# Performance work log

Measured on AMD Instinct MI355X. Metric: run time of the kernel, lower is better.

Reference implementation:

```python
import jax, jax.numpy as jnp
import numpy as np

N_IN = 512    # input nodes occupy indices [0, N_IN)
N_OUT = 256   # output nodes are the last N_OUT node indices


def setup_inputs() -> dict:
    key = jax.random.key(0)
    ks = jax.random.split(key, 7)
    B, N, E = 32, 50000, 800000
    x = jax.random.normal(ks[0], (B, N_IN), dtype=jnp.float32)
    states = jax.random.normal(ks[1], (B, N), dtype=jnp.float32)
    # per-edge scalar weights (NEAT connection genes)
    weight = 0.1 * jax.random.normal(ks[2], (E,), dtype=jnp.float32)
    # per-node scalar bias / response (NEAT node genes)
    bias = 0.1 * jax.random.normal(ks[3], (N,), dtype=jnp.float32)
    response = 1.0 + 0.1 * jax.random.normal(ks[4], (N,), dtype=jnp.float32)
    edge_src = jax.random.randint(ks[5], (E,), 0, N, dtype=jnp.int64) if jax.config.jax_enable_x64 else jax.random.randint(ks[5], (E,), 0, N).astype(jnp.int32)
    edge_dst = jax.random.randint(ks[6], (E,), 0, N, dtype=jnp.int64) if jax.config.jax_enable_x64 else jax.random.randint(ks[6], (E,), 0, N).astype(jnp.int32)
    return {"x": x, "states": states, "weight": weight, "bias": bias,
            "response": response, "edge_src": edge_src, "edge_dst": edge_dst}


def reference(x, states, weight, bias, response, edge_src, edge_dst):
    """One recurrent step of a wired (NEAT-style) RNN.

    For every node i:  z_i = tanh(bias_i + response_i * sum_{(j->i)} w_ji * s_j)
    Input nodes are then clamped to the external input x; outputs are the
    activations of the last N_OUT nodes. Returns (y, new_states) like
    WiredRNN.forward.
    """
    B, N = states.shape
    # gather source states per edge and apply scalar edge weights: [B, E]
    contrib = states[:, edge_src] * weight
    # sum-aggregate incoming messages per destination node: [B, N]
    agg = jnp.zeros((B, N), dtype=states.dtype).at[:, edge_dst].add(contrib)
    z = jnp.tanh(bias + response * agg)
    new_states = z.at[:, :N_IN].set(x)  # input nodes carry the external input
    y = new_states[:, -N_OUT:]
    return (y, new_states)
```

## Files before the change

### kernel.cpp

```cpp
#include <hip/hip_runtime.h>


#define BATCH 32
#define N_IN 512
#define N_OUT 256
#define RB_LOG 6
#define RB 64
#define CAPL 2048
#define MAXR 2048
#define PCH 8192

static __device__ __forceinline__ unsigned short f2bf(float f) {
    unsigned u = __float_as_uint(f);
    unsigned r = (u + 0x7fffu + ((u >> 16) & 1u)) >> 16;
    return (unsigned short)r;
}

__global__ __launch_bounds__(1024)
void fpart_kernel(const float* __restrict__ s, unsigned short* __restrict__ sTb,
                  int N, int PB,
                  const int* __restrict__ edge_src,
                  const int* __restrict__ edge_dst,
                  const float* __restrict__ weight,
                  int* __restrict__ cursors,
                  int2* __restrict__ staging,
                  int E, int R, int CAP) {
    __shared__ int shbuf[4224];
    int tid = threadIdx.x;
    if ((int)blockIdx.x >= PB) {
        float* tiles = (float*)shbuf;
        int tx = tid & 31;
        int ty = tid >> 5;
        int nb = ((int)blockIdx.x - PB) * 128;
#pragma unroll
        for (int t = 0; t < 4; ++t) {
            int n = nb + t * 32 + tx;
            tiles[t * 1056 + ty * 33 + tx] =
                (n < N) ? s[(size_t)ty * N + n] : 0.f;
        }
        __syncthreads();
#pragma unroll
        for (int t = 0; t < 4; ++t) {
            int nn = nb + t * 32 + ty;
            if (nn < N)
                sTb[(size_t)nn * 32 + tx] = f2bf(tiles[t * 1056 + tx * 33 + ty]);
        }
        return;
    }
    int* h    = shbuf;
    int* lcur = shbuf + MAXR;
    for (int i = tid; i < R; i += 1024) h[i] = 0;
    __syncthreads();
    int e0 = blockIdx.x * PCH;
    int e1 = min(e0 + PCH, E);
    int dd[8], ss[8]; float ww[8];
#pragma unroll
    for (int it = 0; it < 2; ++it) {
        int e = e0 + it * 4096 + tid * 4;
#pragma unroll
        for (int j = 0; j < 4; ++j) dd[it * 4 + j] = -1;
        if (e + 4 <= e1) {
            int4 d4 = *reinterpret_cast<const int4*>(edge_dst + e);
            int4 s4 = *reinterpret_cast<const int4*>(edge_src + e);
            float4 w4 = *reinterpret_cast<const float4*>(weight + e);
            dd[it*4+0]=d4.x; dd[it*4+1]=d4.y; dd[it*4+2]=d4.z; dd[it*4+3]=d4.w;
            ss[it*4+0]=s4.x; ss[it*4+1]=s4.y; ss[it*4+2]=s4.z; ss[it*4+3]=s4.w;
            ww[it*4+0]=w4.x; ww[it*4+1]=w4.y; ww[it*4+2]=w4.z; ww[it*4+3]=w4.w;
        } else {
#pragma unroll
            for (int j = 0; j < 4; ++j) {
                if (e + j < e1) {
                    dd[it*4+j] = edge_dst[e + j];
                    ss[it*4+j] = edge_src[e + j];
                    ww[it*4+j] = weight[e + j];
                }
            }
        }
#pragma unroll
        for (int j = 0; j < 4; ++j) {
            int idx = it * 4 + j;
            if (dd[idx] >= N_IN) atomicAdd(&h[dd[idx] >> RB_LOG], 1);
        }
    }
    __syncthreads();
    for (int i = tid; i < R; i += 1024) {
        int c = h[i];
        lcur[i] = c ? (i * CAP + atomicAdd(&cursors[i], c)) : 0;
    }
    __syncthreads();
#pragma unroll
    for (int idx = 0; idx < 8; ++idx) {
        if (dd[idx] >= N_IN) {
            int rng = dd[idx] >> RB_LOG;
            int pos = atomicAdd(&lcur[rng], 1);
            if (pos < (rng + 1) * CAP)
                staging[pos] = make_int2(((dd[idx] & (RB - 1)) << 16) | ss[idx],
                                         __float_as_int(ww[idx]));
        }
    }
}

__global__ __launch_bounds__(512)
void accfin_kernel(const unsigned short* __restrict__ sTb,
                   const int2* __restrict__ staging,
                   const int* __restrict__ cursors,
                   const float* __restrict__ x,
                   const float* __restrict__ bias,
                   const float* __restrict__ response,
                   float* __restrict__ ns, float* __restrict__ y,
                   int N, int CAP) {
    __shared__ float acc[RB * 33];
    __shared__ int2  sorted[CAPL];
    __shared__ int   hstart[RB];
    __shared__ int   hcur[RB];
    int tid = threadIdx.x;
    int r = blockIdx.x;
    int base = r * RB;
    for (int i = tid; i < RB * 33; i += 512) acc[i] = 0.f;

    int b0 = r * CAP;
    int b1 = b0 + min(cursors[r], CAP);
    int q = tid & 7;
    int p = (tid >> 3) & 7;
    int wid = tid >> 6;
    int lane = tid & 63;

    for (int t = b0; t < b1; t += CAPL) {
        int m = min(CAPL, b1 - t);
        if (tid < RB) hstart[tid] = 0;
        __syncthreads();
        for (int i = tid; i < m; i += 512)
            atomicAdd(&hstart[((unsigned)staging[t + i].x) >> 16], 1);
        __syncthreads();
        if (tid < 64) {
            int v = hstart[lane];
            int incl = v;
#pragma unroll
            for (int off = 1; off < 64; off <<= 1) {
                int tv = __shfl_up(incl, off, 64);
                if (lane >= off) incl += tv;
            }
            hstart[lane] = incl - v;
            hcur[lane]   = incl - v;
        }
        __syncthreads();
        for (int i = tid; i < m; i += 512) {
            int2 rc = staging[t + i];
            int pos = atomicAdd(&hcur[((unsigned)rc.x) >> 16], 1);
            sorted[pos] = rc;
        }
        __syncthreads();
#pragma unroll
        for (int k = 0; k < 8; ++k) {
            int nl = wid * 8 + k;
            int beg = hstart[nl], end = hcur[nl];
            float a0 = 0.f, a1 = 0.f, a2 = 0.f, a3 = 0.f;
            for (int e = beg + p; e < end; e += 8) {
                int2 rc = sorted[e];
                float w = __int_as_float(rc.y);
                uint2 u2 = *reinterpret_cast<const uint2*>(
                    sTb + (size_t)(rc.x & 0xffff) * 32 + 4 * q);
                a0 += w * __uint_as_float(u2.x << 16);
                a1 += w * __uint_as_float(u2.x & 0xffff0000u);
                a2 += w * __uint_as_float(u2.y << 16);
                a3 += w * __uint_as_float(u2.y & 0xffff0000u);
            }
#pragma unroll
            for (int off = 8; off < 64; off <<= 1) {
                a0 += __shfl_xor(a0, off, 64);
                a1 += __shfl_xor(a1, off, 64);
                a2 += __shfl_xor(a2, off, 64);
                a3 += __shfl_xor(a3, off, 64);
            }
            if (lane < 8) {
                float* ap = &acc[nl * 33 + 4 * q];
                ap[0] += a0; ap[1] += a1; ap[2] += a2; ap[3] += a3;
            }
        }
        __syncthreads();
    }

    for (int v = tid; v < RB * BATCH; v += 512) {
        int nl = v & (RB - 1);
        int b  = v >> RB_LOG;
        int node = base + nl;
        if (node >= N) continue;
        float val;
        if (node < N_IN)
            val = x[b * N_IN + node];
        else
            val = tanhf(bias[node] + response[node] * acc[nl * 33 + b]);
        ns[(size_t)b * N + node] = val;
        int k = node - (N - N_OUT);
        if (k >= 0) y[b * N_OUT + k] = val;
    }
}

__global__ void edge_kernel_fb(const float* __restrict__ states,
                               const float* __restrict__ weight,
                               const int* __restrict__ edge_src,
                               const int* __restrict__ edge_dst,
                               float* __restrict__ agg, int E, int N) {
    int e = blockIdx.x * blockDim.x + threadIdx.x;
    if (e >= E) return;
    int s = edge_src[e];
    int d = edge_dst[e];
    float w = weight[e];
#pragma unroll
    for (int b = 0; b < BATCH; ++b)
        atomicAdd(agg + (size_t)b * N + d, w * states[(size_t)b * N + s]);
}

__global__ void finish_kernel_fb(const float* __restrict__ x,
                                 const float* __restrict__ agg,
                                 const float* __restrict__ bias,
                                 const float* __restrict__ response,
                                 float* __restrict__ y, float* __restrict__ ns,
                                 int N) {
    int n = blockIdx.x * blockDim.x + threadIdx.x;
    int b = blockIdx.y;
    if (n >= N) return;
    float v;
    if (n < N_IN) v = x[b * N_IN + n];
    else          v = tanhf(bias[n] + response[n] * agg[(size_t)b * N + n]);
    ns[(size_t)b * N + n] = v;
    int n0 = N - N_OUT;
    if (n >= n0) y[b * N_OUT + (n - n0)] = v;
}

extern "C" void kernel_launch(void* const* d_in, const int* in_sizes, int n_in,
                              void* d_out, int out_size, void* d_ws, size_t ws_size,
                              hipStream_t stream) {
    const float* x        = (const float*)d_in[0];
    const float* states   = (const float*)d_in[1];
    const float* weight   = (const float*)d_in[2];
    const float* bias     = (const float*)d_in[3];
    const float* response = (const float*)d_in[4];
    const int*   edge_src = (const int*)d_in[5];
    const int*   edge_dst = (const int*)d_in[6];

    int N = in_sizes[3];
    int E = in_sizes[5];

    float* y  = (float*)d_out;
    float* ns = (float*)d_out + BATCH * N_OUT;

    int tgrid4 = (N + 127) / 128;
    int R  = (N + RB - 1) / RB;
    int PB = (E + PCH - 1) / PCH;

    int mean = (E + R - 1) / R;
    int CAP  = ((4 * mean + CAPL - 1) / CAPL) * CAPL;

    size_t staging_bytes = ((size_t)R * CAP * 8 + 15) & ~(size_t)15;
    size_t sTb_bytes     = ((size_t)N * 32 * 2 + 15) & ~(size_t)15;
    size_t cur_bytes     = ((size_t)R * 4 + 15) & ~(size_t)15;
    size_t needed = staging_bytes + sTb_bytes + cur_bytes + 64;

    if (ws_size < needed || R > MAXR || N > 65536) {
        float* agg = (float*)d_ws;
        hipMemsetAsync(agg, 0, (size_t)BATCH * N * sizeof(float), stream);
        int egrid = (E + 255) / 256;
        edge_kernel_fb<<<egrid, 256, 0, stream>>>(states, weight, edge_src,
                                                  edge_dst, agg, E, N);
        dim3 fgrid((N + 255) / 256, BATCH);
        finish_kernel_fb<<<fgrid, 256, 0, stream>>>(x, agg, bias, response,
                                                    y, ns, N);
        return;
    }

    char* p = (char*)d_ws;
    int2*           staging = (int2*)p;           p += staging_bytes;
    unsigned short* sTb     = (unsigned short*)p; p += sTb_bytes;
    int*            cursors = (int*)p;

    hipMemsetAsync(cursors, 0, (size_t)R * 4, stream);

    fpart_kernel<<<PB + tgrid4, 1024, 0, stream>>>(
        states, sTb, N, PB, edge_src, edge_dst, weight,
        cursors, staging, E, R, CAP);

    accfin_kernel<<<R, 512, 0, stream>>>(sTb, staging, cursors, x,
                                         bias, response, ns, y, N, CAP);
}
```

Measured before the change: 46.26 us.

## Fuse partition and accumulate kernels into one cooperative kernel with grid sync

```diff
diff --git a/kernel.cpp b/kernel.cpp
--- a/kernel.cpp
+++ b/kernel.cpp
@@ -1,4 +1,5 @@
 #include <hip/hip_runtime.h>
+#include <hip/hip_cooperative_groups.h>
 
 
 #define BATCH 32
@@ -8,12 +9,211 @@
 #define RB 64
 #define CAPL 2048
 #define MAXR 2048
-#define PCH 8192
+#define PCHC 4096
+#define PCHF 8192
+#define SMEM_INTS 6336
 
 static __device__ __forceinline__ unsigned short f2bf(float f) {
     unsigned u = __float_as_uint(f);
     unsigned r = (u + 0x7fffu + ((u >> 16) & 1u)) >> 16;
     return (unsigned short)r;
+}
+
+__global__ __launch_bounds__(512, 8)
+void fused_kernel(const float* __restrict__ s,
+                  unsigned short* __restrict__ sTb,
+                  const int* __restrict__ edge_src,
+                  const int* __restrict__ edge_dst,
+                  const float* __restrict__ weight,
+                  int* __restrict__ cursors,
+                  int2* __restrict__ staging,
+                  const float* __restrict__ x,
+                  const float* __restrict__ bias,
+                  const float* __restrict__ response,
+                  float* __restrict__ ns, float* __restrict__ y,
+                  int N, int E, int R, int CAP, int PB, int TG) {
+    __shared__ int smem[SMEM_INTS];
+    int tid = threadIdx.x;
+    int bid = blockIdx.x;
+
+    if (bid < PB) {
+        int* h    = smem;
+        int* lcur = smem + R;
+        for (int i = tid; i < R; i += 512) h[i] = 0;
+        __syncthreads();
+        int e0 = bid * PCHC;
+        int e1 = min(e0 + PCHC, E);
+        int dd[8], ss[8]; float ww[8];
+#pragma unroll
+        for (int it = 0; it < 2; ++it) {
+            int e = e0 + it * 2048 + tid * 4;
+#pragma unroll
+            for (int j = 0; j < 4; ++j) dd[it * 4 + j] = -1;
+            if (e + 4 <= e1) {
+                int4 d4 = *reinterpret_cast<const int4*>(edge_dst + e);
+                int4 s4 = *reinterpret_cast<const int4*>(edge_src + e);
+                float4 w4 = *reinterpret_cast<const float4*>(weight + e);
+                dd[it*4+0]=d4.x; dd[it*4+1]=d4.y; dd[it*4+2]=d4.z; dd[it*4+3]=d4.w;
+                ss[it*4+0]=s4.x; ss[it*4+1]=s4.y; ss[it*4+2]=s4.z; ss[it*4+3]=s4.w;
+                ww[it*4+0]=w4.x; ww[it*4+1]=w4.y; ww[it*4+2]=w4.z; ww[it*4+3]=w4.w;
+            } else {
+#pragma unroll
+                for (int j = 0; j < 4; ++j) {
+                    if (e + j < e1) {
+                        dd[it*4+j] = edge_dst[e + j];
+                        ss[it*4+j] = edge_src[e + j];
+                        ww[it*4+j] = weight[e + j];
+                    }
+                }
+            }
+#pragma unroll
+            for (int j = 0; j < 4; ++j) {
+                int idx = it * 4 + j;
+                if (dd[idx] >= N_IN) atomicAdd(&h[dd[idx] >> RB_LOG], 1);
+            }
+        }
+        __syncthreads();
+        for (int i = tid; i < R; i += 512) {
+            int c = h[i];
+            lcur[i] = c ? (i * CAP + atomicAdd(&cursors[i], c)) : 0;
+        }
+        __syncthreads();
+#pragma unroll
+        for (int idx = 0; idx < 8; ++idx) {
+            if (dd[idx] >= N_IN) {
+                int rng = dd[idx] >> RB_LOG;
+                int pos = atomicAdd(&lcur[rng], 1);
+                if (pos < (rng + 1) * CAP)
+                    staging[pos] = make_int2(((dd[idx] & (RB - 1)) << 16) | ss[idx],
+                                             __float_as_int(ww[idx]));
+            }
+        }
+    } else if (bid < PB + TG) {
+        float* tiles = (float*)smem;
+        int tx = tid & 31;
+        int ty0 = tid >> 5;
+        int nb = (bid - PB) * 128;
+#pragma unroll
+        for (int t = 0; t < 4; ++t)
+            for (int b = ty0; b < 32; b += 16) {
+                int n = nb + t * 32 + tx;
+                tiles[t * 1056 + b * 33 + tx] =
+                    (n < N) ? s[(size_t)b * N + n] : 0.f;
+            }
+        __syncthreads();
+#pragma unroll
+        for (int t = 0; t < 4; ++t)
+            for (int nn0 = ty0; nn0 < 32; nn0 += 16) {
+                int nn = nb + t * 32 + nn0;
+                if (nn < N)
+                    sTb[(size_t)nn * 32 + tx] = f2bf(tiles[t * 1056 + tx * 33 + nn0]);
+            }
+    }
+
+    cooperative_groups::this_grid().sync();
+
+    {
+        int r = bid;
+        int base = r * RB;
+        float* acc    = (float*)smem;
+        int2*  sorted = (int2*)(smem + RB * 33);
+        int*   hstart = smem + RB * 33 + 2 * CAPL;
+        int*   hcur   = hstart + RB;
+
+        for (int i = tid; i < RB * 33; i += 512) acc[i] = 0.f;
+
+        int b0 = r * CAP;
+        int b1 = b0 + min(cursors[r], CAP);
+        int q = tid & 7;
+        int p = (tid >> 3) & 7;
+        int wid = tid >> 6;
+        int lane = tid & 63;
+
+        for (int t = b0; t < b1; t += CAPL) {
+            int m = min(CAPL, b1 - t);
+            if (tid < RB) hstart[tid] = 0;
+            __syncthreads();
+            int2 rc[4];
+            int rb = tid * 4;
+            if (rb + 4 <= m) {
+                const int4* sp = reinterpret_cast<const int4*>(&staging[t + rb]);
+                int4 a = sp[0], b = sp[1];
+                rc[0] = make_int2(a.x, a.y); rc[1] = make_int2(a.z, a.w);
+                rc[2] = make_int2(b.x, b.y); rc[3] = make_int2(b.z, b.w);
+            } else {
+#pragma unroll
+                for (int j = 0; j < 4; ++j)
+                    if (rb + j < m) rc[j] = staging[t + rb + j];
+            }
+#pragma unroll
+            for (int j = 0; j < 4; ++j)
+                if (rb + j < m)
+                    atomicAdd(&hstart[((unsigned)rc[j].x) >> 16], 1);
+            __syncthreads();
+            if (tid < 64) {
+                int v = hstart[lane];
+                int incl = v;
+#pragma unroll
+                for (int off = 1; off < 64; off <<= 1) {
+                    int tv = __shfl_up(incl, off, 64);
+                    if (lane >= off) incl += tv;
+                }
+                hstart[lane] = incl - v;
+                hcur[lane]   = incl - v;
+            }
+            __syncthreads();
+#pragma unroll
+            for (int j = 0; j < 4; ++j)
+                if (rb + j < m) {
+                    int pos = atomicAdd(&hcur[((unsigned)rc[j].x) >> 16], 1);
+                    sorted[pos] = rc[j];
+                }
+            __syncthreads();
+#pragma unroll
+            for (int k = 0; k < 8; ++k) {
+                int nl = wid * 8 + k;
+                int beg = hstart[nl], end = hcur[nl];
+                float a0 = 0.f, a1 = 0.f, a2 = 0.f, a3 = 0.f;
+                for (int e = beg + p; e < end; e += 8) {
+                    int2 rcv = sorted[e];
+                    float w = __int_as_float(rcv.y);
+                    uint2 u2 = *reinterpret_cast<const uint2*>(
+                        sTb + (size_t)(rcv.x & 0xffff) * 32 + 4 * q);
+                    a0 += w * __uint_as_float(u2.x << 16);
+                    a1 += w * __uint_as_float(u2.x & 0xffff0000u);
+                    a2 += w * __uint_as_float(u2.y << 16);
+                    a3 += w * __uint_as_float(u2.y & 0xffff0000u);
+                }
+#pragma unroll
+                for (int off = 8; off < 64; off <<= 1) {
+                    a0 += __shfl_xor(a0, off, 64);
+                    a1 += __shfl_xor(a1, off, 64);
+                    a2 += __shfl_xor(a2, off, 64);
+                    a3 += __shfl_xor(a3, off, 64);
+                }
+                if (lane < 8) {
+                    float* ap = &acc[nl * 33 + 4 * q];
+                    ap[0] += a0; ap[1] += a1; ap[2] += a2; ap[3] += a3;
+                }
+            }
+            __syncthreads();
+        }
+
+        for (int v = tid; v < RB * BATCH; v += 512) {
+            int nl = v & (RB - 1);
+            int b  = v >> RB_LOG;
+            int node = base + nl;
+            if (node >= N) continue;
+            float val;
+            if (node < N_IN)
+                val = x[b * N_IN + node];
+            else
+                val = tanhf(bias[node] + response[node] * acc[nl * 33 + b]);
+            ns[(size_t)b * N + node] = val;
+            int k = node - (N - N_OUT);
+            if (k >= 0) y[b * N_OUT + k] = val;
+        }
+    }
 }
 
 __global__ __launch_bounds__(1024)
@@ -35,8 +235,7 @@
 #pragma unroll
         for (int t = 0; t < 4; ++t) {
             int n = nb + t * 32 + tx;
-            tiles[t * 1056 + ty * 33 + tx] =
-                (n < N) ? s[(size_t)ty * N + n] : 0.f;
+            tiles[t * 1056 + ty * 33 + tx] = (n < N) ? s[(size_t)ty * N + n] : 0.f;
         }
         __syncthreads();
 #pragma unroll
@@ -51,8 +250,8 @@
     int* lcur = shbuf + MAXR;
     for (int i = tid; i < R; i += 1024) h[i] = 0;
     __syncthreads();
-    int e0 = blockIdx.x * PCH;
-    int e1 = min(e0 + PCH, E);
+    int e0 = blockIdx.x * PCHF;
+    int e1 = min(e0 + PCHF, E);
     int dd[8], ss[8]; float ww[8];
 #pragma unroll
     for (int it = 0; it < 2; ++it) {
@@ -117,14 +316,12 @@
     int r = blockIdx.x;
     int base = r * RB;
     for (int i = tid; i < RB * 33; i += 512) acc[i] = 0.f;
-
     int b0 = r * CAP;
     int b1 = b0 + min(cursors[r], CAP);
     int q = tid & 7;
     int p = (tid >> 3) & 7;
     int wid = tid >> 6;
     int lane = tid & 63;
-
     for (int t = b0; t < b1; t += CAPL) {
         int m = min(CAPL, b1 - t);
         if (tid < RB) hstart[tid] = 0;
@@ -179,7 +376,6 @@
         }
         __syncthreads();
     }
-
     for (int v = tid; v < RB * BATCH; v += 512) {
         int nl = v & (RB - 1);
         int b  = v >> RB_LOG;
@@ -231,13 +427,13 @@
 extern "C" void kernel_launch(void* const* d_in, const int* in_sizes, int n_in,
                               void* d_out, int out_size, void* d_ws, size_t ws_size,
                               hipStream_t stream) {
-    const float* x        = (const float*)d_in[0];
     const float* states   = (const float*)d_in[1];
     const float* weight   = (const float*)d_in[2];
     const float* bias     = (const float*)d_in[3];
     const float* response = (const float*)d_in[4];
     const int*   edge_src = (const int*)d_in[5];
     const int*   edge_dst = (const int*)d_in[6];
+    const float* x        = (const float*)d_in[0];
 
     int N = in_sizes[3];
     int E = in_sizes[5];
@@ -245,9 +441,10 @@
     float* y  = (float*)d_out;
     float* ns = (float*)d_out + BATCH * N_OUT;
 
-    int tgrid4 = (N + 127) / 128;
-    int R  = (N + RB - 1) / RB;
-    int PB = (E + PCH - 1) / PCH;
+    int R   = (N + RB - 1) / RB;
+    int TG  = (N + 127) / 128;
+    int PBc = (E + PCHC - 1) / PCHC;
+    int PBf = (E + PCHF - 1) / PCHF;
 
     int mean = (E + R - 1) / R;
     int CAP  = ((4 * mean + CAPL - 1) / CAPL) * CAPL;
@@ -276,10 +473,33 @@
 
     hipMemsetAsync(cursors, 0, (size_t)R * 4, stream);
 
-    fpart_kernel<<<PB + tgrid4, 1024, 0, stream>>>(
-        states, sTb, N, PB, edge_src, edge_dst, weight,
+    bool coop = (PBc + TG <= R) && (2 * R <= SMEM_INTS);
+    int dev = 0, cus = 0, blocksPerCu = 0;
+    if (coop && hipGetDevice(&dev) == hipSuccess &&
+        hipDeviceGetAttribute(&cus, hipDeviceAttributeMultiprocessorCount,
+                              dev) == hipSuccess &&
+        hipOccupancyMaxActiveBlocksPerMultiprocessor(
+            &blocksPerCu, fused_kernel, 512, 0) == hipSuccess) {
+        coop = (blocksPerCu * cus >= R);
+    } else {
+        coop = false;
+    }
+
+    if (coop) {
+        void* args[] = {
+            (void*)&states, (void*)&sTb, (void*)&edge_src, (void*)&edge_dst,
+            (void*)&weight, (void*)&cursors, (void*)&staging, (void*)&x,
+            (void*)&bias, (void*)&response, (void*)&ns, (void*)&y,
+            (void*)&N, (void*)&E, (void*)&R, (void*)&CAP,
+            (void*)&PBc, (void*)&TG};
+        hipError_t err = hipLaunchCooperativeKernel(
+            (const void*)fused_kernel, dim3(R), dim3(512), args, 0, stream);
+        if (err == hipSuccess) return;
+    }
+
+    fpart_kernel<<<PBf + TG, 1024, 0, stream>>>(
+        states, sTb, N, PBf, edge_src, edge_dst, weight,
         cursors, staging, E, R, CAP);
-
     accfin_kernel<<<R, 512, 0, stream>>>(sTb, staging, cursors, x,
                                          bias, response, ns, y, N, CAP);
 }
```

Result: no change. 46.50 us (+0.5%).
